# Performance work log

Measured on AMD Instinct MI355X. Metric: run time of the kernel, lower is better.

Reference implementation:

```python
import jax, jax.numpy as jnp
import numpy as np

H = 128           # hidden_size
N_NODE = 100000   # item vocab
B = 1024          # sessions
NODES_PER = 50
N = B * NODES_PER # total session nodes
E = 8 * N         # edges


def setup_inputs() -> dict:
    key = jax.random.key(0)
    ks = jax.random.split(key, 16)
    stdv = 1.0 / np.sqrt(H)
    u = lambda k, shape: jax.random.uniform(k, shape, jnp.float32, -stdv, stdv)
    x = jax.random.randint(ks[0], (N,), 1, N_NODE + 1)      # 1-indexed items
    edge_index = jax.random.randint(ks[1], (2, E), 0, N)
    batch = jnp.repeat(jnp.arange(B), NODES_PER)            # sorted segment ids
    return {
        "x": x, "edge_index": edge_index, "batch": batch,
        "emb_weight": u(ks[2], (N_NODE, H)),
        "W_gconv": u(ks[3], (H, H)),
        "W_ih": u(ks[4], (3 * H, H)), "W_hh": u(ks[5], (3 * H, H)),
        "b_ih": u(ks[6], (3 * H,)), "b_hh": u(ks[7], (3 * H,)),
        "W1_w": u(ks[8], (H, H)), "W1_b": u(ks[9], (H,)),
        "W2_w": u(ks[10], (H, H)), "W2_b": u(ks[11], (H,)),
        "q_w": u(ks[12], (1, H)), "q_b": u(ks[13], (1,)),
        "W3_w": u(ks[14], (H, 2 * H)), "W3_b": u(ks[15], (H,)),
    }


def _forward(x, edge_index, batch, emb_weight, W_gconv, W_ih, W_hh, b_ih, b_hh,
             W1_w, W1_b, W2_w, W2_b, q_w, q_b, W3_w, W3_b):
    n = x.shape[0]
    h = emb_weight[x - 1]                                   # [N, H]
    # GatedGraphConv, num_layers=1: linear -> scatter-add -> GRUCell
    m = h @ W_gconv                                          # [N, H]
    agg = jax.ops.segment_sum(m[edge_index[0]], edge_index[1], num_segments=n)
    gi = agg @ W_ih.T + b_ih                                 # [N, 3H]
    gh = h @ W_hh.T + b_hh
    i_r, i_z, i_n = jnp.split(gi, 3, axis=1)
    h_r, h_z, h_n = jnp.split(gh, 3, axis=1)
    r = jax.nn.sigmoid(i_r + h_r)
    z = jax.nn.sigmoid(i_z + h_z)
    ng = jnp.tanh(i_n + r * h_n)
    h = (1.0 - z) * ng + z * h
    h = jax.nn.relu(h)
    # Embedding2Score: segment-wise attention readout
    last_idx = jax.ops.segment_max(jnp.arange(n), batch, num_segments=B)
    v_n = h[last_idx]                                        # [B, H] last node per session
    a = jax.nn.sigmoid(v_n[batch] @ W1_w.T + W1_b + h @ W2_w.T + W2_b)
    alpha = a @ q_w.T + q_b                                  # [N, 1]
    s_g = jax.ops.segment_sum(alpha * h, batch, num_segments=B)  # [B, H]
    s_h = jnp.concatenate([v_n, s_g], axis=1) @ W3_w.T + W3_b    # [B, H]
    return s_h @ emb_weight.T                                # [B, n_node]


def reference(x, edge_index, batch, emb_weight, W_gconv, W_ih, W_hh, b_ih, b_hh,
              W1_w, W1_b, W2_w, W2_b, q_w, q_b, W3_w, W3_b):
    return _forward(x, edge_index, batch, emb_weight, W_gconv, W_ih, W_hh, b_ih, b_hh,
                    W1_w, W1_b, W2_w, W2_b, q_w, q_b, W3_w, W3_b)
```

## Files before the change

kernel.cpp:

```cpp
#include <hip/hip_runtime.h>
#include <math.h>

#define NNODES 51200
#define NEDGES 409600
#define NB 1024
#define NODES_PER 50
#define NVOCAB 100000
#define NVPAD 100096
#define SLOTS 64

typedef __attribute__((ext_vector_type(8))) short bf16x8;
typedef __attribute__((ext_vector_type(4))) float f32x4;

__device__ __forceinline__ float sigf(float x) { return 1.0f / (1.0f + __expf(-x)); }

__device__ __forceinline__ ushort f2bf(float x) {
    union { float f; unsigned u; } v; v.f = x;
    const unsigned r = v.u + 0x7FFF + ((v.u >> 16) & 1);
    return (ushort)(r >> 16);
}
__device__ __forceinline__ float bf2f(ushort u) {
    union { float f; unsigned u; } v; v.u = ((unsigned)u) << 16; return v.f;
}
__device__ __forceinline__ bf16x8 cvt8(const float* __restrict__ src) {
    const float4 v0 = *(const float4*)src, v1 = *(const float4*)(src + 4);
    bf16x8 p;
    p[0] = (short)f2bf(v0.x); p[1] = (short)f2bf(v0.y);
    p[2] = (short)f2bf(v0.z); p[3] = (short)f2bf(v0.w);
    p[4] = (short)f2bf(v1.x); p[5] = (short)f2bf(v1.y);
    p[6] = (short)f2bf(v1.z); p[7] = (short)f2bf(v1.w);
    return p;
}

__global__ __launch_bounds__(256)
void prep_kernel(const int* __restrict__ x, const float* __restrict__ emb,
                 ushort* __restrict__ hb, const int* __restrict__ ei,
                 int* __restrict__ cnt, int* __restrict__ esrc,
                 ushort* __restrict__ embswz, const float* __restrict__ Wih,
                 const float* __restrict__ Wg, ushort* __restrict__ Wc,
                 const float* __restrict__ Whh, ushort* __restrict__ Whhb,
                 const float* __restrict__ W2, ushort* __restrict__ W2b) {
    const int bid = blockIdx.x;
    const int t = threadIdx.x;
    if (bid < 3200) {
        const int tid = bid * 256 + t;
        const int i = tid >> 4, c8 = (tid & 15) * 8;
        const int idx = x[i] - 1;
        *(bf16x8*)(hb + (size_t)i * 128 + c8) = cvt8(emb + (size_t)idx * 128 + c8);
    } else if (bid < 4800) {
        const int e = (bid - 3200) * 256 + t;
        const int dst = ei[NEDGES + e];
        const int pos = atomicAdd(&cnt[dst], 1);
        if (pos < SLOTS) esrc[(size_t)dst * SLOTS + pos] = ei[e];
    } else if (bid < 11056) {
        const int f = (bid - 4800) * 256 + t;
        const int row = f >> 4, c8 = (f & 15) * 8;
        bf16x8 pk = {0, 0, 0, 0, 0, 0, 0, 0};
        if (row < NVOCAB) pk = cvt8(emb + (size_t)row * 128 + c8);
        *(bf16x8*)&embswz[(size_t)row * 128 + (c8 ^ ((row & 7) << 3))] = pk;
    } else if (bid < 11248) {
        const int idx = (bid - 11056) * 256 + t;
        const int mrow = idx >> 7, n = idx & 127;
        const float* wr = Wih + (size_t)mrow * 128;
        const float* gr = Wg + (size_t)n * 128;
        float acc = 0.f;
        #pragma unroll 8
        for (int k = 0; k < 128; ++k)
            acc = fmaf(wr[k], gr[k], acc);
        Wc[mrow * 128 + (n ^ ((mrow & 7) << 3))] = f2bf(acc);
    } else if (bid < 11272) {
        const int f = (bid - 11248) * 256 + t;
        const int r = f >> 4, c8 = (f & 15) * 8;
        *(bf16x8*)&Whhb[r * 128 + (c8 ^ ((r & 7) << 3))] = cvt8(Whh + (size_t)r * 128 + c8);
    } else {
        const int f = (bid - 11272) * 256 + t;
        const int r = f >> 4, c8 = (f & 15) * 8;
        *(bf16x8*)&W2b[r * 128 + (c8 ^ ((r & 7) << 3))] = cvt8(W2 + (size_t)r * 128 + c8);
    }
}

__global__ __launch_bounds__(256)
void agg_kernel(const int* __restrict__ cnt, const int* __restrict__ esrc,
                const ushort* __restrict__ hb, ushort* __restrict__ aggb) {
    const int node = blockIdx.x * 4 + (threadIdx.x >> 6);
    const int l = threadIdx.x & 63;
    int cn = cnt[node]; if (cn > SLOTS) cn = SLOTS;
    const int* es = esrc + (size_t)node * SLOTS;
    float ax = 0.f, ay = 0.f;
    for (int j = 0; j < cn; ++j) {
        const int src = es[j];
        const unsigned u = *(const unsigned*)(hb + (size_t)src * 128 + l * 2);
        ax += bf2f((ushort)(u & 0xffff));
        ay += bf2f((ushort)(u >> 16));
    }
    const unsigned o = (unsigned)f2bf(ax) | ((unsigned)f2bf(ay) << 16);
    *(unsigned*)(aggb + (size_t)node * 128 + ((l * 2) ^ ((node & 7) << 3))) = o;
}

__global__ __launch_bounds__(512)
void gru_fused(const ushort* __restrict__ aggb, const ushort* __restrict__ Wc,
               const ushort* __restrict__ Whhb, const float* __restrict__ bih,
               const float* __restrict__ bhh, ushort* __restrict__ hb) {
    __shared__ ushort As[128 * 128];
    __shared__ ushort Bs[384 * 128];
    const int m0 = blockIdx.x * 128;
    const int t = threadIdx.x;
    const int lane = t & 63, wid = t >> 6;
    const int l15 = lane & 15, kg = (lane >> 4) * 8;

    #pragma unroll
    for (int f = t; f < 2048; f += 512)
        *(bf16x8*)&As[f * 8] = *(const bf16x8*)(aggb + (size_t)m0 * 128 + f * 8);
    #pragma unroll
    for (int f = t; f < 6144; f += 512)
        *(bf16x8*)&Bs[f * 8] = *(const bf16x8*)(Wc + (size_t)f * 8);
    __syncthreads();

    f32x4 gi[24] = {};
    #pragma unroll
    for (int kc = 0; kc < 4; ++kc) {
        const int cs = kc * 32 + kg;
        const int ra = wid * 16 + l15;
        const bf16x8 af = *(const bf16x8*)&As[ra * 128 + (cs ^ ((ra & 7) << 3))];
        #pragma unroll
        for (int j = 0; j < 24; ++j) {
            const int rb = j * 16 + l15;
            const bf16x8 bfr = *(const bf16x8*)&Bs[rb * 128 + (cs ^ ((rb & 7) << 3))];
            gi[j] = __builtin_amdgcn_mfma_f32_16x16x32_bf16(af, bfr, gi[j], 0, 0, 0);
        }
    }
    __syncthreads();

    #pragma unroll
    for (int f = t; f < 2048; f += 512) {
        const int r = f >> 4, c8 = (f & 15) * 8;
        const bf16x8 pk = *(const bf16x8*)(hb + (size_t)(m0 + r) * 128 + c8);
        *(bf16x8*)&As[r * 128 + (c8 ^ ((r & 7) << 3))] = pk;
    }
    #pragma unroll
    for (int f = t; f < 6144; f += 512)
        *(bf16x8*)&Bs[f * 8] = *(const bf16x8*)(Whhb + (size_t)f * 8);
    __syncthreads();

    f32x4 gh[24] = {};
    #pragma unroll
    for (int kc = 0; kc < 4; ++kc) {
        const int cs = kc * 32 + kg;
        const int ra = wid * 16 + l15;
        const bf16x8 af = *(const bf16x8*)&As[ra * 128 + (cs ^ ((ra & 7) << 3))];
        #pragma unroll
        for (int j = 0; j < 24; ++j) {
            const int rb = j * 16 + l15;
            const bf16x8 bfr = *(const bf16x8*)&Bs[rb * 128 + (cs ^ ((rb & 7) << 3))];
            gh[j] = __builtin_amdgcn_mfma_f32_16x16x32_bf16(af, bfr, gh[j], 0, 0, 0);
        }
    }

    const int lr0 = wid * 16 + (lane >> 4) * 4;
    #pragma unroll
    for (int j = 0; j < 8; ++j) {
        const int col = j * 16 + l15;
        const float bir = bih[col], biz = bih[128 + col], bin = bih[256 + col];
        const float bhr = bhh[col], bhz = bhh[128 + col], bhn = bhh[256 + col];
        #pragma unroll
        for (int q = 0; q < 4; ++q) {
            const int lr = lr0 + q;
            const int adr = lr * 128 + (col ^ ((lr & 7) << 3));
            const float hv = bf2f(As[adr]);
            const float r_ = sigf(gi[j][q] + bir + gh[j][q] + bhr);
            const float z  = sigf(gi[j + 8][q] + biz + gh[j + 8][q] + bhz);
            const float ng = tanhf(gi[j + 16][q] + bin + r_ * (gh[j + 16][q] + bhn));
            As[adr] = f2bf(fmaxf((1.f - z) * ng + z * hv, 0.f));
        }
    }
    __syncthreads();
    #pragma unroll
    for (int f = t; f < 2048; f += 512) {
        const int r = f >> 4, c8 = (f & 15) * 8;
        *(bf16x8*)(hb + (size_t)(m0 + r) * 128 + c8) =
            *(const bf16x8*)&As[r * 128 + (c8 ^ ((r & 7) << 3))];
    }
}

__global__ __launch_bounds__(256)
void attn_sh(const ushort* __restrict__ hb, const float* __restrict__ W1,
             const float* __restrict__ b1, const ushort* __restrict__ W2b,
             const float* __restrict__ qw, const float* __restrict__ qbp,
             const float* __restrict__ b2, const float* __restrict__ W3,
             const float* __restrict__ b3, ushort* __restrict__ shb) {
    __shared__ ushort As[128 * 128];
    __shared__ ushort Bs[128 * 128];
    __shared__ float t1s[2][128];
    __shared__ float qws[128];
    __shared__ float apar[2][2][64];
    __shared__ float alph[2][64];
    __shared__ float sgs[2][128];
    const int m0 = blockIdx.x * 100;
    const int t = threadIdx.x;
    const int lane = t & 63, wid = t >> 6;
    const int wr = wid >> 1, wc = wid & 1;
    const int l15 = lane & 15, kg = (lane >> 4) * 8;
    const int cr0 = (lane >> 4) * 4;

    #pragma unroll
    for (int f = t; f < 2048; f += 256) {
        const int r = f >> 4, c8 = (f & 15) * 8;
        int gr = m0 + r; if (gr > NNODES - 1) gr = NNODES - 1;
        *(bf16x8*)&As[r * 128 + (c8 ^ ((r & 7) << 3))] =
            *(const bf16x8*)(hb + (size_t)gr * 128 + c8);
        *(bf16x8*)&Bs[f * 8] = *(const bf16x8*)(W2b + (size_t)f * 8);
    }
    if (t < 128) qws[t] = qw[t];
    __syncthreads();

    f32x4 acc[4][4] = {};
    #pragma unroll
    for (int kc = 0; kc < 4; ++kc) {
        const int cs = kc * 32 + kg;
        bf16x8 af[4], bfr[4];
        #pragma unroll
        for (int i = 0; i < 4; ++i) {
            const int ra = wr * 64 + i * 16 + l15;
            af[i] = *(const bf16x8*)&As[ra * 128 + (cs ^ ((ra & 7) << 3))];
            const int rb = wc * 64 + i * 16 + l15;
            bfr[i] = *(const bf16x8*)&Bs[rb * 128 + (cs ^ ((rb & 7) << 3))];
        }
        #pragma unroll
        for (int i = 0; i < 4; ++i)
            #pragma unroll
            for (int j = 0; j < 4; ++j)
                acc[i][j] = __builtin_amdgcn_mfma_f32_16x16x32_bf16(af[i], bfr[j], acc[i][j], 0, 0, 0);
    }
    __syncthreads();

    #pragma unroll
    for (int j = 0; j < 4; ++j) {
        const int col = wc * 64 + j * 16 + l15;
        const int csw = (col & 7) << 3;
        #pragma unroll
        for (int i = 0; i < 4; ++i) {
            const int row = wr * 64 + i * 16 + cr0;
            #pragma unroll
            for (int q = 0; q < 4; ++q)
                Bs[col * 128 + ((row + q) ^ csw)] = f2bf(acc[i][j][q]);
        }
    }

    const int sess = wid >> 1, half = wid & 1;
    const int d = half * 64 + lane;
    const int vrow = sess * 50 + 49;
    const int vsw = (vrow & 7) << 3;
    float t1v = b1[d] + b2[d];
    const float* w1r = W1 + (size_t)d * 128;
    #pragma unroll 8
    for (int k = 0; k < 128; k += 4) {
        const float4 w = *(const float4*)(w1r + k);
        t1v += w.x * bf2f(As[vrow * 128 + ((k + 0) ^ vsw)])
             + w.y * bf2f(As[vrow * 128 + ((k + 1) ^ vsw)])
             + w.z * bf2f(As[vrow * 128 + ((k + 2) ^ vsw)])
             + w.w * bf2f(As[vrow * 128 + ((k + 3) ^ vsw)]);
    }
    t1s[sess][d] = t1v;
    __syncthreads();

    float p = 0.f;
    if (lane < 50) {
        const int row = sess * 50 + lane;
        const int d0 = half * 64;
        #pragma unroll 8
        for (int dd = d0; dd < d0 + 64; ++dd)
            p += qws[dd] * sigf(t1s[sess][dd] + bf2f(Bs[dd * 128 + (row ^ ((dd & 7) << 3))]));
    }
    apar[sess][half][lane] = p;
    __syncthreads();
    if (half == 0 && lane < 50)
        alph[sess][lane] = apar[sess][0][lane] + apar[sess][1][lane] + qbp[0];
    __syncthreads();

    float sacc = 0.f;
    #pragma unroll 10
    for (int i = 0; i < 50; ++i) {
        const int row = sess * 50 + i;
        sacc += alph[sess][i] * bf2f(As[row * 128 + (d ^ ((row & 7) << 3))]);
    }
    sgs[sess][d] = sacc;
    __syncthreads();

    float shacc = b3[d];
    const float* w3r = W3 + (size_t)d * 256;
    #pragma unroll 8
    for (int k = 0; k < 128; k += 4) {
        const float4 w = *(const float4*)(w3r + k);
        shacc += w.x * bf2f(As[vrow * 128 + ((k + 0) ^ vsw)])
               + w.y * bf2f(As[vrow * 128 + ((k + 1) ^ vsw)])
               + w.z * bf2f(As[vrow * 128 + ((k + 2) ^ vsw)])
               + w.w * bf2f(As[vrow * 128 + ((k + 3) ^ vsw)]);
    }
    #pragma unroll 8
    for (int k = 0; k < 128; k += 4) {
        const float4 w = *(const float4*)(w3r + 128 + k);
        shacc += w.x * sgs[sess][k] + w.y * sgs[sess][k + 1]
               + w.z * sgs[sess][k + 2] + w.w * sgs[sess][k + 3];
    }
    const int orow = blockIdx.x * 2 + sess;
    shb[(size_t)orow * 128 + (d ^ ((orow & 7) << 3))] = f2bf(shacc);
}

__global__ __launch_bounds__(256)
void gemm_vocab(float* __restrict__ C, const ushort* __restrict__ Ab,
                const ushort* __restrict__ Bswz) {
    __shared__ ushort As[128 * 128];
    __shared__ ushort Bs[128 * 128];
    float* Cs = (float*)Bs;
    const int id = blockIdx.x;
    const int xcd = id & 7, loc = id >> 3;
    const int mt = loc & 7, g = loc >> 3;
    const int grp = xcd * 49 + g;
    if (grp * 256 >= NVOCAB) return;
    const int m0 = mt * 128;
    const int t = threadIdx.x;
    const int lane = t & 63, wid = t >> 6;
    const int wr = wid >> 1, wc = wid & 1;
    const int l15 = lane & 15, kg = (lane >> 4) * 8;
    const int cr0 = (lane >> 4) * 4;

    #pragma unroll
    for (int f = t; f < 2048; f += 256)
        *(bf16x8*)&As[f * 8] = *(const bf16x8*)(Ab + (size_t)m0 * 128 + f * 8);

    for (int it = 0; it < 2; ++it) {
        const int n0 = (grp * 2 + it) * 128;
        if (n0 >= NVOCAB) break;
        __syncthreads();
        const ushort* srcb = Bswz + (size_t)n0 * 128;
        #pragma unroll
        for (int f = t; f < 2048; f += 256)
            *(bf16x8*)&Bs[f * 8] = *(const bf16x8*)(srcb + f * 8);
        __syncthreads();

        f32x4 acc[4][4] = {};
        #pragma unroll
        for (int kc = 0; kc < 4; ++kc) {
            const int cs = kc * 32 + kg;
            bf16x8 af[4], bfr[4];
            #pragma unroll
            for (int i = 0; i < 4; ++i) {
                const int ra = wr * 64 + i * 16 + l15;
                af[i] = *(const bf16x8*)&As[ra * 128 + (cs ^ ((ra & 7) << 3))];
                const int rb = wc * 64 + i * 16 + l15;
                bfr[i] = *(const bf16x8*)&Bs[rb * 128 + (cs ^ ((rb & 7) << 3))];
            }
            #pragma unroll
            for (int i = 0; i < 4; ++i)
                #pragma unroll
                for (int j = 0; j < 4; ++j)
                    acc[i][j] = __builtin_amdgcn_mfma_f32_16x16x32_bf16(af[i], bfr[j], acc[i][j], 0, 0, 0);
        }
        __syncthreads();

        #pragma unroll
        for (int half = 0; half < 2; ++half) {
            if (wr == half) {
                #pragma unroll
                for (int j = 0; j < 4; ++j) {
                    const int col = wc * 64 + j * 16 + l15;
                    #pragma unroll
                    for (int i = 0; i < 4; ++i) {
                        const int rl = i * 16 + cr0;
                        #pragma unroll
                        for (int q = 0; q < 4; ++q)
                            Cs[(rl + q) * 128 + col] = acc[i][j][q];
                    }
                }
            }
            __syncthreads();
            #pragma unroll
            for (int f = t; f < 2048; f += 256) {
                const int r = f >> 5, c4 = (f & 31) * 4;
                if (n0 + c4 < NVOCAB) {
                    const f32x4 v = *(const f32x4*)&Cs[r * 128 + c4];
                    *(f32x4*)(C + (size_t)(m0 + half * 64 + r) * NVOCAB + n0 + c4) = v;
                }
            }
            __syncthreads();
        }
    }
}

extern "C" void kernel_launch(void* const* d_in, const int* in_sizes, int n_in,
                              void* d_out, int out_size, void* d_ws, size_t ws_size,
                              hipStream_t stream) {
    const int*   x   = (const int*)d_in[0];
    const int*   ei  = (const int*)d_in[1];
    const float* emb = (const float*)d_in[3];
    const float* Wg  = (const float*)d_in[4];
    const float* Wih = (const float*)d_in[5];
    const float* Whh = (const float*)d_in[6];
    const float* bih = (const float*)d_in[7];
    const float* bhh = (const float*)d_in[8];
    const float* W1  = (const float*)d_in[9];
    const float* b1  = (const float*)d_in[10];
    const float* W2  = (const float*)d_in[11];
    const float* b2  = (const float*)d_in[12];
    const float* qw  = (const float*)d_in[13];
    const float* qb  = (const float*)d_in[14];
    const float* W3  = (const float*)d_in[15];
    const float* b3  = (const float*)d_in[16];
    float* out = (float*)d_out;

    float*  ws     = (float*)d_ws;
    ushort* hb     = (ushort*)ws;
    ushort* aggb   = (ushort*)(ws + 3276800);
    ushort* Wc     = (ushort*)(ws + 6553600);
    ushort* Whhb   = (ushort*)(ws + 6578176);
    ushort* W2b    = (ushort*)(ws + 6602752);
    ushort* shb    = (ushort*)(ws + 6610944);
    ushort* embswz = (ushort*)(ws + 6676480);
    int*    cnt    = (int*)(ws + 13082624);
    int*    esrc   = cnt + NNODES;

    hipMemsetAsync(cnt, 0, NNODES * sizeof(int), stream);

    prep_kernel<<<11280, 256, 0, stream>>>(x, emb, hb, ei, cnt, esrc, embswz,
                                           Wih, Wg, Wc, Whh, Whhb, W2, W2b);

    agg_kernel<<<12800, 256, 0, stream>>>(cnt, esrc, hb, aggb);

    gru_fused<<<400, 512, 0, stream>>>(aggb, Wc, Whhb, bih, bhh, hb);

    attn_sh<<<512, 256, 0, stream>>>(hb, W1, b1, W2b, qw, qb, b2, W3, b3, shb);

    gemm_vocab<<<3136, 256, 0, stream>>>(out, shb, embswz);
}
```

Baseline: 315.9 us.

## Give each vocab GEMM block a single 128-column tile and write the full tile at once

The vocab GEMM now assigns one 128x128 output tile per block instead of two sequential N tiles, doubling the grid to 6272 blocks. Shared memory is merged into one 64KB buffer so the full 128x128 fp32 C tile can be staged and written in one pass, not in two halves with extra barriers. This aims to raise parallelism and cut barrier count in the output-write-bound kernel. In exchange the A tile is reloaded per block, and the larger LDS footprint per block may lower occupancy.

```diff
diff --git a/kernel.cpp b/kernel.cpp
--- a/kernel.cpp
+++ b/kernel.cpp
@@ -309,14 +309,15 @@
 __global__ __launch_bounds__(256)
 void gemm_vocab(float* __restrict__ C, const ushort* __restrict__ Ab,
                 const ushort* __restrict__ Bswz) {
-    __shared__ ushort As[128 * 128];
-    __shared__ ushort Bs[128 * 128];
-    float* Cs = (float*)Bs;
+    __shared__ ushort smem[2 * 128 * 128];
+    ushort* As = smem;
+    ushort* Bs = smem + 128 * 128;
+    float* Cs = (float*)smem;
     const int id = blockIdx.x;
-    const int xcd = id & 7, loc = id >> 3;
-    const int mt = loc & 7, g = loc >> 3;
-    const int grp = xcd * 49 + g;
-    if (grp * 256 >= NVOCAB) return;
+    const int xcd = id & 7, mt = (id >> 3) & 7, g = id >> 6;
+    const int grp = xcd * 98 + g;
+    if (grp >= 782) return;
+    const int n0 = grp * 128;
     const int m0 = mt * 128;
     const int t = threadIdx.x;
     const int lane = t & 63, wid = t >> 6;
@@ -324,65 +325,54 @@
     const int l15 = lane & 15, kg = (lane >> 4) * 8;
     const int cr0 = (lane >> 4) * 4;
 
-    #pragma unroll
-    for (int f = t; f < 2048; f += 256)
-        *(bf16x8*)&As[f * 8] = *(const bf16x8*)(Ab + (size_t)m0 * 128 + f * 8);
-
-    for (int it = 0; it < 2; ++it) {
-        const int n0 = (grp * 2 + it) * 128;
-        if (n0 >= NVOCAB) break;
-        __syncthreads();
-        const ushort* srcb = Bswz + (size_t)n0 * 128;
-        #pragma unroll
-        for (int f = t; f < 2048; f += 256)
-            *(bf16x8*)&Bs[f * 8] = *(const bf16x8*)(srcb + f * 8);
-        __syncthreads();
-
-        f32x4 acc[4][4] = {};
-        #pragma unroll
-        for (int kc = 0; kc < 4; ++kc) {
-            const int cs = kc * 32 + kg;
-            bf16x8 af[4], bfr[4];
+    const ushort* srca = Ab + (size_t)m0 * 128;
+    const ushort* srcb = Bswz + (size_t)n0 * 128;
+    #pragma unroll
+    for (int f = t; f < 2048; f += 256) {
+        *(bf16x8*)&As[f * 8] = *(const bf16x8*)(srca + f * 8);
+        *(bf16x8*)&Bs[f * 8] = *(const bf16x8*)(srcb + f * 8);
+    }
+    __syncthreads();
+
+    f32x4 acc[4][4] = {};
+    #pragma unroll
+    for (int kc = 0; kc < 4; ++kc) {
+        const int cs = kc * 32 + kg;
+        bf16x8 af[4], bfr[4];
+        #pragma unroll
+        for (int i = 0; i < 4; ++i) {
+            const int ra = wr * 64 + i * 16 + l15;
+            af[i] = *(const bf16x8*)&As[ra * 128 + (cs ^ ((ra & 7) << 3))];
+            const int rb = wc * 64 + i * 16 + l15;
+            bfr[i] = *(const bf16x8*)&Bs[rb * 128 + (cs ^ ((rb & 7) << 3))];
+        }
+        #pragma unroll
+        for (int i = 0; i < 4; ++i)
             #pragma unroll
-            for (int i = 0; i < 4; ++i) {
-                const int ra = wr * 64 + i * 16 + l15;
-                af[i] = *(const bf16x8*)&As[ra * 128 + (cs ^ ((ra & 7) << 3))];
-                const int rb = wc * 64 + i * 16 + l15;
-                bfr[i] = *(const bf16x8*)&Bs[rb * 128 + (cs ^ ((rb & 7) << 3))];
-            }
+            for (int j = 0; j < 4; ++j)
+                acc[i][j] = __builtin_amdgcn_mfma_f32_16x16x32_bf16(af[i], bfr[j], acc[i][j], 0, 0, 0);
+    }
+    __syncthreads();
+
+    #pragma unroll
+    for (int j = 0; j < 4; ++j) {
+        const int col = wc * 64 + j * 16 + l15;
+        #pragma unroll
+        for (int i = 0; i < 4; ++i) {
+            const int row = wr * 64 + i * 16 + cr0;
             #pragma unroll
-            for (int i = 0; i < 4; ++i)
-                #pragma unroll
-                for (int j = 0; j < 4; ++j)
-                    acc[i][j] = __builtin_amdgcn_mfma_f32_16x16x32_bf16(af[i], bfr[j], acc[i][j], 0, 0, 0);
-        }
-        __syncthreads();
-
-        #pragma unroll
-        for (int half = 0; half < 2; ++half) {
-            if (wr == half) {
-                #pragma unroll
-                for (int j = 0; j < 4; ++j) {
-                    const int col = wc * 64 + j * 16 + l15;
-                    #pragma unroll
-                    for (int i = 0; i < 4; ++i) {
-                        const int rl = i * 16 + cr0;
-                        #pragma unroll
-                        for (int q = 0; q < 4; ++q)
-                            Cs[(rl + q) * 128 + col] = acc[i][j][q];
-                    }
-                }
-            }
-            __syncthreads();
-            #pragma unroll
-            for (int f = t; f < 2048; f += 256) {
-                const int r = f >> 5, c4 = (f & 31) * 4;
-                if (n0 + c4 < NVOCAB) {
-                    const f32x4 v = *(const f32x4*)&Cs[r * 128 + c4];
-                    *(f32x4*)(C + (size_t)(m0 + half * 64 + r) * NVOCAB + n0 + c4) = v;
-                }
-            }
-            __syncthreads();
+            for (int q = 0; q < 4; ++q)
+                Cs[(row + q) * 128 + col] = acc[i][j][q];
+        }
+    }
+    __syncthreads();
+
+    #pragma unroll
+    for (int f = t; f < 4096; f += 256) {
+        const int r = f >> 5, c4 = (f & 31) * 4;
+        if (n0 + c4 < NVOCAB) {
+            const f32x4 v = *(const f32x4*)&Cs[r * 128 + c4];
+            *(f32x4*)(C + (size_t)(m0 + r) * NVOCAB + n0 + c4) = v;
         }
     }
 }
@@ -430,5 +420,5 @@
 
     attn_sh<<<512, 256, 0, stream>>>(hb, W1, b1, W2b, qw, qb, b2, W3, b3, shb);
 
-    gemm_vocab<<<3136, 256, 0, stream>>>(out, shb, embswz);
-}
+    gemm_vocab<<<6272, 256, 0, stream>>>(out, shb, embswz);
+}
```

After: 310.3 us. About the same (-1.8%).
